# Optimization experiments

Hardware: AMD Instinct MI355X
Metric: run time of the kernel (lower is better)

## Reference

```python
import jax, jax.numpy as jnp
import numpy as np

SEGMENT_LENGTHS = [2048, 4096]
DILATION_RATES = [1, 2]


def _group_attention(qg, kg, vg, seg_len, r, gidx):
    # qg/kg/vg: [b, gh, n, d]; segmented dilated attention for one head group.
    b, gh, n, d = qg.shape
    nseg = n // seg_len
    scale = float(1.0 / np.sqrt(d))
    qs = qg.reshape(b, gh, nseg, seg_len, d)
    ks = kg.reshape(b, gh, nseg, seg_len, d)
    vs = vg.reshape(b, gh, nseg, seg_len, d)
    if r > 1:
        m = seg_len // r
        # offset = (group_idx + seg_idx) % r; pattern = offset + r*arange(m) (no wrap since seg_len % r == 0)
        offsets = (gidx + jnp.arange(nseg)) % r            # [nseg]
        idx = offsets[:, None] + r * jnp.arange(m)[None, :]  # [nseg, m]
        si = jnp.arange(nseg)[:, None]                      # [nseg, 1]
        qd = qs[:, :, si, idx]                              # [b, gh, nseg, m, d]
        kd = ks[:, :, si, idx]
        vd = vs[:, :, si, idx]
    else:
        qd, kd, vd = qs, ks, vs
    scores = jnp.einsum('bgsqd,bgskd->bgsqk', qd, kd) * scale
    attn = jax.nn.softmax(scores, axis=-1)
    out = jnp.einsum('bgsqk,bgskd->bgsqd', attn, vd)
    if r > 1:
        # scatter dilated outputs back to their segment positions; unselected positions stay 0
        full = jnp.zeros((b, gh, nseg, seg_len, d), dtype=qg.dtype)
        out = full.at[:, :, si, idx].set(out)
    return out.reshape(b, gh, n, d)


def reference(q, k, v):
    # q, k, v: [b, n, h, d]; ring_size == 1 -> single-device dilated attention
    b, n, h, d = q.shape
    ngroups = len(SEGMENT_LENGTHS)
    gsize = h // ngroups
    qt = jnp.transpose(q, (0, 2, 1, 3))  # [b, h, n, d]
    kt = jnp.transpose(k, (0, 2, 1, 3))
    vt = jnp.transpose(v, (0, 2, 1, 3))
    outs = []
    for i, (s, r) in enumerate(zip(SEGMENT_LENGTHS, DILATION_RATES)):
        hs, he = i * gsize, (i + 1) * gsize
        outs.append(_group_attention(qt[:, hs:he], kt[:, hs:he], vt[:, hs:he], s, r, i))
    out = jnp.concatenate(outs, axis=1)   # [b, h, n, d]
    return jnp.transpose(out, (0, 2, 1, 3))  # [b, n, h, d]


def setup_inputs() -> dict:
    key = jax.random.key(0)
    kq, kk, kv = jax.random.split(key, 3)
    shape = (1, 8192, 16, 128)
    return {
        'q': jax.random.normal(kq, shape, dtype=jnp.float32),
        'k': jax.random.normal(kk, shape, dtype=jnp.float32),
        'v': jax.random.normal(kv, shape, dtype=jnp.float32),
    }
```

## Files before the change

### kernel.cpp

```cpp
#include <hip/hip_runtime.h>
#include <hip/hip_bf16.h>

typedef __attribute__((ext_vector_type(8)))  short bf16x8;
typedef __attribute__((ext_vector_type(4)))  float f32x4;
typedef __attribute__((ext_vector_type(16))) float f32x16;
typedef __attribute__((ext_vector_type(4)))  int   int4v;

__device__ __forceinline__ short f2bf(float f) {
    unsigned u = __builtin_bit_cast(unsigned, f);
    unsigned r = u + 0x7fffu + ((u >> 16) & 1u);
    return (short)(r >> 16);
}

__device__ __forceinline__ int row_map(int p, int j) {
    if (p < 32) return (p & 3) * 2048 + j;
    return ((p - 32) & 1) == 0 ? (2 * j + 1) : (4096 + 2 * j);
}
__device__ __forceinline__ int head_of(int p) {
    return (p < 32) ? (p >> 2) : (8 + ((p - 32) >> 1));
}

__global__ __launch_bounds__(256) void conv_k_kernel(
    const float* __restrict__ K, short* __restrict__ Kws)
{
    const int cid = blockIdx.x * 256 + threadIdx.x;
    const int p   = cid >> 15;
    const int rem = cid & 32767;
    const int row = rem >> 4;
    const int d8  = (rem & 15) << 3;
    const int g   = row_map(p, row);
    const float* src = K + ((size_t)(g * 16 + head_of(p))) * 128 + d8;
    bf16x8 o;
    #pragma unroll
    for (int e = 0; e < 8; ++e) o[e] = f2bf(src[e]);
    *(bf16x8*)(Kws + (((size_t)p * 2048 + row) << 7) + d8) = o;
}

__global__ __launch_bounds__(256) void conv_v_kernel(
    const float* __restrict__ V, short* __restrict__ Vws)
{
    __shared__ short T[128][72];
    const int p  = blockIdx.x >> 5;
    const int kb = blockIdx.x & 31;
    const int tid = threadIdx.x;
    const int h = head_of(p);
    #pragma unroll
    for (int it = 0; it < 4; ++it) {
        const int cid  = it * 256 + tid;
        const int krow = cid & 63;
        const int d8   = (cid >> 6) << 3;
        const int g = row_map(p, kb * 64 + krow);
        const float* vp = V + ((size_t)(g * 16 + h)) * 128 + d8;
        #pragma unroll
        for (int e = 0; e < 8; ++e) T[d8 + e][krow] = f2bf(vp[e]);
    }
    __syncthreads();
    #pragma unroll
    for (int it = 0; it < 4; ++it) {
        const int j   = it * 256 + tid;
        const int d   = j >> 3;
        const int c16 = j & 7;
        bf16x8 val = *(const bf16x8*)&T[d][c16 * 8];
        *(bf16x8*)(Vws + ((size_t)p * 128 + d) * 2048 + kb * 64 + c16 * 8) = val;
    }
}

__global__ __launch_bounds__(256, 2) void dilated_attn7_kernel(
    const float* __restrict__ Q, const short* __restrict__ Kws,
    const short* __restrict__ Vws, float* __restrict__ O)
{
    __shared__ short Ks[64 * 128];
    __shared__ short Vt[128 * 64];
    __shared__ float sbuf[4][32];

    const int logical = (blockIdx.x & 7) * 96 + (blockIdx.x >> 3);
    const int pid  = logical >> 4;
    const int tile = logical & 15;
    const int h    = head_of(pid);

    const int tid  = threadIdx.x;
    const int wave = tid >> 6;
    const int lane = tid & 63;
    const int ql   = lane & 31;
    const int hi   = lane >> 5;

    const float scale_log2e = 0.08838834764831845f * 1.4426950408889634f;

    const short* Kp = Kws + ((size_t)pid * 2048 << 7);
    const short* Vp = Vws + ((size_t)pid * 128) * 2048;

    bf16x8 qf[8];
    {
        const int j = tile * 128 + wave * 32 + ql;
        const int g = row_map(pid, j);
        const float* qp = Q + ((size_t)(g * 16 + h)) * 128 + hi * 8;
        #pragma unroll
        for (int c = 0; c < 8; ++c) {
            bf16x8 f;
            #pragma unroll
            for (int e = 0; e < 8; ++e) f[e] = f2bf(qp[c * 16 + e] * scale_log2e);
            qf[c] = f;
        }
    }

    f32x16 oacc[4];
    #pragma unroll
    for (int dt = 0; dt < 4; ++dt) oacc[dt] = (f32x16)0.f;
    float m = -3.0e38f, l = 0.f;

    int4v kreg[4], vreg[4];

    auto LOADR = [&](int kb) {
        #pragma unroll
        for (int it = 0; it < 4; ++it) {
            const int j   = it * 256 + wave * 64 + lane;
            const int row = j >> 4;
            const int u   = j & 15;
            kreg[it] = *(const int4v*)(Kp + (((size_t)(kb * 64 + row)) << 7) + u * 8);
        }
        #pragma unroll
        for (int it = 0; it < 4; ++it) {
            const int j   = it * 256 + wave * 64 + lane;
            const int row = j >> 3;
            const int u   = j & 7;
            vreg[it] = *(const int4v*)(Vp + (size_t)row * 2048 + kb * 64 + u * 8);
        }
    };
    auto WRITE = [&]() {
        #pragma unroll
        for (int it = 0; it < 4; ++it) {
            const int j   = it * 256 + wave * 64 + lane;
            const int row = j >> 4;
            const int u   = j & 15;
            *(int4v*)&Ks[row * 128 + ((u ^ (row & 15)) << 3)] = kreg[it];
        }
        #pragma unroll
        for (int it = 0; it < 4; ++it) {
            const int j   = it * 256 + wave * 64 + lane;
            const int row = j >> 3;
            const int u   = j & 7;
            *(int4v*)&Vt[row * 64 + ((u ^ (row & 7)) << 3)] = vreg[it];
        }
    };

    LOADR(0);
    WRITE();
    __syncthreads();

    for (int t = 0; t < 32; ++t) {
        if (t < 31) LOADR(t + 1);

        f32x16 p[2];
        #pragma unroll
        for (int kt2 = 0; kt2 < 2; ++kt2) {
            f32x16 acc = (f32x16)0.f;
            const int row = kt2 * 32 + ql;
            #pragma unroll
            for (int c = 0; c < 8; ++c) {
                const int u = 2 * c + hi;
                bf16x8 a = *(const bf16x8*)&Ks[row * 128 + ((u ^ (row & 15)) << 3)];
                acc = __builtin_amdgcn_mfma_f32_32x32x16_bf16(a, qf[c], acc, 0, 0, 0);
            }
            p[kt2] = acc;
        }

        float rm = p[0][0];
        #pragma unroll
        for (int kt2 = 0; kt2 < 2; ++kt2)
            #pragma unroll
            for (int r = 0; r < 16; ++r) rm = fmaxf(rm, p[kt2][r]);
        rm = fmaxf(rm, __shfl_xor(rm, 32));

        if (__any(rm > m + 8.0f)) {
            const float mn = fmaxf(m, rm);
            const float sf = exp2f(m - mn);
            m = mn;
            l *= sf;
            if (lane < 32) sbuf[wave][lane] = sf;
            #pragma unroll
            for (int r = 0; r < 16; ++r) {
                const float s = sbuf[wave][(r & 3) + 8 * (r >> 2) + 4 * hi];
                #pragma unroll
                for (int dt = 0; dt < 4; ++dt) oacc[dt][r] *= s;
            }
        }

        float rs = 0.f;
        #pragma unroll
        for (int kt2 = 0; kt2 < 2; ++kt2)
            #pragma unroll
            for (int r = 0; r < 16; ++r) {
                const float pv = exp2f(p[kt2][r] - m);
                p[kt2][r] = pv;
                rs += pv;
            }
        rs += __shfl_xor(rs, 32);
        l += rs;

        bf16x8 pa[4];
        #pragma unroll
        for (int kt2 = 0; kt2 < 2; ++kt2) {
            int A0, A1, B0, B1, C0, C1, D0, D1;
            asm("v_cvt_pk_bf16_f32 %0,%1,%2" : "=v"(A0) : "v"(p[kt2][0]),  "v"(p[kt2][1]));
            asm("v_cvt_pk_bf16_f32 %0,%1,%2" : "=v"(A1) : "v"(p[kt2][2]),  "v"(p[kt2][3]));
            asm("v_cvt_pk_bf16_f32 %0,%1,%2" : "=v"(B0) : "v"(p[kt2][4]),  "v"(p[kt2][5]));
            asm("v_cvt_pk_bf16_f32 %0,%1,%2" : "=v"(B1) : "v"(p[kt2][6]),  "v"(p[kt2][7]));
            asm("v_cvt_pk_bf16_f32 %0,%1,%2" : "=v"(C0) : "v"(p[kt2][8]),  "v"(p[kt2][9]));
            asm("v_cvt_pk_bf16_f32 %0,%1,%2" : "=v"(C1) : "v"(p[kt2][10]), "v"(p[kt2][11]));
            asm("v_cvt_pk_bf16_f32 %0,%1,%2" : "=v"(D0) : "v"(p[kt2][12]), "v"(p[kt2][13]));
            asm("v_cvt_pk_bf16_f32 %0,%1,%2" : "=v"(D1) : "v"(p[kt2][14]), "v"(p[kt2][15]));
            asm("v_permlane32_swap_b32 %0, %1" : "+v"(A0), "+v"(B0));
            asm("v_permlane32_swap_b32 %0, %1" : "+v"(A1), "+v"(B1));
            asm("v_permlane32_swap_b32 %0, %1" : "+v"(C0), "+v"(D0));
            asm("v_permlane32_swap_b32 %0, %1" : "+v"(C1), "+v"(D1));
            pa[2 * kt2 + 0] = __builtin_bit_cast(bf16x8, (int4v){A0, A1, B0, B1});
            pa[2 * kt2 + 1] = __builtin_bit_cast(bf16x8, (int4v){C0, C1, D0, D1});
        }

        #pragma unroll
        for (int ks = 0; ks < 4; ++ks) {
            #pragma unroll
            for (int dt = 0; dt < 4; ++dt) {
                const int row = dt * 32 + ql;
                const int u   = 2 * ks + hi;
                bf16x8 vb = *(const bf16x8*)&Vt[row * 64 + ((u ^ (row & 7)) << 3)];
                oacc[dt] = __builtin_amdgcn_mfma_f32_32x32x16_bf16(pa[ks], vb, oacc[dt], 0, 0, 0);
            }
        }

        if (t < 31) {
            __syncthreads();
            WRITE();
            __syncthreads();
        }
    }

    if (lane < 32) sbuf[wave][lane] = 1.f / l;
    #pragma unroll
    for (int r = 0; r < 16; ++r) {
        const int qrow = (r & 3) + 8 * (r >> 2) + 4 * hi;
        const float inv = sbuf[wave][qrow];
        const int j = tile * 128 + wave * 32 + qrow;
        const int g = row_map(pid, j);
        float* op = O + ((size_t)(g * 16 + h)) * 128 + ql;
        #pragma unroll
        for (int dt = 0; dt < 4; ++dt)
            op[dt * 32] = oacc[dt][r] * inv;
    }
}

__global__ __launch_bounds__(256) void zero_fill_kernel(float* __restrict__ O)
{
    const int t = blockIdx.x * 256 + threadIdx.x;
    const int c4   = t & 31;
    const int rowi = (t >> 5) & 4095;
    const int hh   = t >> 17;
    const int row  = (rowi < 2048) ? (2 * rowi) : (4096 + 2 * (rowi - 2048) + 1);
    float4 z; z.x = 0.f; z.y = 0.f; z.z = 0.f; z.w = 0.f;
    *(float4*)&O[((size_t)(row * 16) + 8 + hh) * 128 + c4 * 4] = z;
}

#define BK    64
#define KPAD  136
#define VPAD  72
__global__ __launch_bounds__(256) void dilated_attn_v1_kernel(
    const float* __restrict__ Q, const float* __restrict__ K,
    const float* __restrict__ V, float* __restrict__ O)
{
    __shared__ short KsL[BK][KPAD];
    __shared__ short VtL[128][VPAD];
    __shared__ short PsL[4][16][VPAD];
    const int bid  = blockIdx.x;
    const int p    = bid >> 5;
    const int tile = bid & 31;
    const int h    = head_of(p);
    const int tid  = threadIdx.x;
    const int wave = tid >> 6;
    const int lane = tid & 63;
    const int lr   = lane & 15;
    const int lg   = lane >> 4;
    const float scale_log2e = 0.08838834764831845f * 1.4426950408889634f;
    bf16x8 qf[4];
    {
        const int j = tile * 64 + wave * 16 + lr;
        const int g = row_map(p, j);
        const float* qp = Q + ((size_t)(g * 16 + h)) * 128 + lg * 8;
        #pragma unroll
        for (int c = 0; c < 4; ++c) {
            bf16x8 f;
            #pragma unroll
            for (int e = 0; e < 8; ++e) f[e] = f2bf(qp[c * 32 + e] * scale_log2e);
            qf[c] = f;
        }
    }
    f32x4 oacc[8];
    #pragma unroll
    for (int i = 0; i < 8; ++i) oacc[i] = (f32x4)0.f;
    float m[4], l[4];
    #pragma unroll
    for (int r = 0; r < 4; ++r) { m[r] = -3.0e38f; l[r] = 0.f; }
    for (int kb = 0; kb < 2048 / BK; ++kb) {
        __syncthreads();
        #pragma unroll
        for (int it = 0; it < 4; ++it) {
            const int cid  = it * 256 + tid;
            const int krow = cid >> 4;
            const int dcol = (cid & 15) << 3;
            const int g = row_map(p, kb * BK + krow);
            const float* kp = K + ((size_t)(g * 16 + h)) * 128 + dcol;
            bf16x8 kk;
            #pragma unroll
            for (int e = 0; e < 8; ++e) kk[e] = f2bf(kp[e]);
            *(bf16x8*)&KsL[krow][dcol] = kk;
        }
        #pragma unroll
        for (int it = 0; it < 4; ++it) {
            const int cid  = it * 256 + tid;
            const int krow = cid & 63;
            const int dcol = (cid >> 6) << 3;
            const int g = row_map(p, kb * BK + krow);
            const float* vp = V + ((size_t)(g * 16 + h)) * 128 + dcol;
            #pragma unroll
            for (int e = 0; e < 8; ++e) VtL[dcol + e][krow] = f2bf(vp[e]);
        }
        __syncthreads();
        f32x4 s[4];
        #pragma unroll
        for (int t = 0; t < 4; ++t) {
            f32x4 acc = (f32x4)0.f;
            #pragma unroll
            for (int c = 0; c < 4; ++c) {
                bf16x8 b = *(const bf16x8*)&KsL[t * 16 + lr][c * 32 + lg * 8];
                acc = __builtin_amdgcn_mfma_f32_16x16x32_bf16(qf[c], b, acc, 0, 0, 0);
            }
            s[t] = acc;
        }
        #pragma unroll
        for (int r = 0; r < 4; ++r) {
            float bm = fmaxf(fmaxf(s[0][r], s[1][r]), fmaxf(s[2][r], s[3][r]));
            bm = fmaxf(bm, __shfl_xor(bm, 1));
            bm = fmaxf(bm, __shfl_xor(bm, 2));
            bm = fmaxf(bm, __shfl_xor(bm, 4));
            bm = fmaxf(bm, __shfl_xor(bm, 8));
            const float mn = fmaxf(m[r], bm);
            const float sf = exp2f(m[r] - mn);
            m[r] = mn;
            float rs = 0.f;
            #pragma unroll
            for (int t = 0; t < 4; ++t) {
                const float pv = exp2f(s[t][r] - mn);
                s[t][r] = pv;
                rs += pv;
            }
            rs += __shfl_xor(rs, 1);
            rs += __shfl_xor(rs, 2);
            rs += __shfl_xor(rs, 4);
            rs += __shfl_xor(rs, 8);
            l[r] = l[r] * sf + rs;
            #pragma unroll
            for (int dt = 0; dt < 8; ++dt) oacc[dt][r] *= sf;
        }
        #pragma unroll
        for (int t = 0; t < 4; ++t)
            #pragma unroll
            for (int r = 0; r < 4; ++r)
                PsL[wave][lg * 4 + r][t * 16 + lr] = f2bf(s[t][r]);
        #pragma unroll
        for (int cc = 0; cc < 2; ++cc) {
            bf16x8 pa = *(const bf16x8*)&PsL[wave][lr][cc * 32 + lg * 8];
            #pragma unroll
            for (int dt = 0; dt < 8; ++dt) {
                bf16x8 vb = *(const bf16x8*)&VtL[dt * 16 + lr][cc * 32 + lg * 8];
                oacc[dt] = __builtin_amdgcn_mfma_f32_16x16x32_bf16(pa, vb, oacc[dt], 0, 0, 0);
            }
        }
    }
    #pragma unroll
    for (int r = 0; r < 4; ++r) {
        const int j = tile * 64 + wave * 16 + lg * 4 + r;
        const int g = row_map(p, j);
        const float inv = 1.f / l[r];
        float* op = O + ((size_t)(g * 16 + h)) * 128 + lr;
        #pragma unroll
        for (int dt = 0; dt < 8; ++dt)
            op[dt * 16] = oacc[dt][r] * inv;
    }
}

extern "C" void kernel_launch(void* const* d_in, const int* in_sizes, int n_in,
                              void* d_out, int out_size, void* d_ws, size_t ws_size,
                              hipStream_t stream) {
    const float* q = (const float*)d_in[0];
    const float* k = (const float*)d_in[1];
    const float* v = (const float*)d_in[2];
    float* o = (float*)d_out;

    const size_t kws_elems = (size_t)48 * 2048 * 128;
    const size_t need = kws_elems * 2 * 2;
    hipLaunchKernelGGL(zero_fill_kernel, dim3(4096), dim3(256), 0, stream, o);
    if (ws_size >= need) {
        short* kws = (short*)d_ws;
        short* vws = kws + kws_elems;
        hipLaunchKernelGGL(conv_k_kernel, dim3(6144), dim3(256), 0, stream, k, kws);
        hipLaunchKernelGGL(conv_v_kernel, dim3(1536), dim3(256), 0, stream, v, vws);
        hipLaunchKernelGGL(dilated_attn7_kernel, dim3(48 * 16), dim3(256), 0, stream,
                           q, kws, vws, o);
    } else {
        hipLaunchKernelGGL(dilated_attn_v1_kernel, dim3(48 * 32), dim3(256), 0, stream,
                           q, k, v, o);
    }
}
```

Baseline: 181.0 us.

## Load V tiles straight into double-buffered LDS via global_load_lds

V tiles now go directly from global memory into a double-buffered LDS array using the global_load_lds builtin, with the XOR swizzle applied on the source address, so they no longer pass through registers. K still uses register staging into a single buffer. This frees vector registers, and launch bounds are raised from 2 to 3 blocks per CU to try for more occupancy. The trade-offs are more LDS per block and a full vmcnt(0) wait before each barrier, which also waits on the K loads.

```diff
diff --git a/kernel.cpp b/kernel.cpp
--- a/kernel.cpp
+++ b/kernel.cpp
@@ -19,6 +19,11 @@
 __device__ __forceinline__ int head_of(int p) {
     return (p < 32) ? (p >> 2) : (8 + ((p - 32) >> 1));
 }
+
+#define GLDS(gsrc, ldst)                                                          \
+    __builtin_amdgcn_global_load_lds(                                             \
+        (const __attribute__((address_space(1))) unsigned int*)(gsrc),            \
+        (__attribute__((address_space(3))) unsigned int*)(ldst), 16, 0, 0)
 
 __global__ __launch_bounds__(256) void conv_k_kernel(
     const float* __restrict__ K, short* __restrict__ Kws)
@@ -65,12 +70,12 @@
     }
 }
 
-__global__ __launch_bounds__(256, 2) void dilated_attn7_kernel(
+__global__ __launch_bounds__(256, 3) void dilated_attn8_kernel(
     const float* __restrict__ Q, const short* __restrict__ Kws,
     const short* __restrict__ Vws, float* __restrict__ O)
 {
     __shared__ short Ks[64 * 128];
-    __shared__ short Vt[128 * 64];
+    __shared__ short Vt[2][128 * 64];
     __shared__ float sbuf[4][32];
 
     const int logical = (blockIdx.x & 7) * 96 + (blockIdx.x >> 3);
@@ -108,9 +113,19 @@
     for (int dt = 0; dt < 4; ++dt) oacc[dt] = (f32x16)0.f;
     float m = -3.0e38f, l = 0.f;
 
-    int4v kreg[4], vreg[4];
-
-    auto LOADR = [&](int kb) {
+    int4v kreg[4];
+
+    auto GLDS_V = [&](int buf, int kb) {
+        #pragma unroll
+        for (int it = 0; it < 4; ++it) {
+            const int j   = it * 256 + wave * 64 + lane;
+            const int row = j >> 3;
+            const int u   = j & 7;
+            GLDS(Vp + (size_t)row * 2048 + kb * 64 + ((u ^ (row & 7)) << 3),
+                 &Vt[buf][(it * 256 + wave * 64) * 8]);
+        }
+    };
+    auto LOADK = [&](int kb) {
         #pragma unroll
         for (int it = 0; it < 4; ++it) {
             const int j   = it * 256 + wave * 64 + lane;
@@ -118,15 +133,8 @@
             const int u   = j & 15;
             kreg[it] = *(const int4v*)(Kp + (((size_t)(kb * 64 + row)) << 7) + u * 8);
         }
-        #pragma unroll
-        for (int it = 0; it < 4; ++it) {
-            const int j   = it * 256 + wave * 64 + lane;
-            const int row = j >> 3;
-            const int u   = j & 7;
-            vreg[it] = *(const int4v*)(Vp + (size_t)row * 2048 + kb * 64 + u * 8);
-        }
     };
-    auto WRITE = [&]() {
+    auto WRITEK = [&]() {
         #pragma unroll
         for (int it = 0; it < 4; ++it) {
             const int j   = it * 256 + wave * 64 + lane;
@@ -134,21 +142,20 @@
             const int u   = j & 15;
             *(int4v*)&Ks[row * 128 + ((u ^ (row & 15)) << 3)] = kreg[it];
         }
-        #pragma unroll
-        for (int it = 0; it < 4; ++it) {
-            const int j   = it * 256 + wave * 64 + lane;
-            const int row = j >> 3;
-            const int u   = j & 7;
-            *(int4v*)&Vt[row * 64 + ((u ^ (row & 7)) << 3)] = vreg[it];
-        }
     };
 
-    LOADR(0);
-    WRITE();
+    GLDS_V(0, 0);
+    LOADK(0);
+    WRITEK();
+    asm volatile("s_waitcnt vmcnt(0)" ::: "memory");
     __syncthreads();
 
     for (int t = 0; t < 32; ++t) {
-        if (t < 31) LOADR(t + 1);
+        const int cur = t & 1;
+        if (t < 31) {
+            GLDS_V(cur ^ 1, t + 1);
+            LOADK(t + 1);
+        }
 
         f32x16 p[2];
         #pragma unroll
@@ -223,14 +230,15 @@
             for (int dt = 0; dt < 4; ++dt) {
                 const int row = dt * 32 + ql;
                 const int u   = 2 * ks + hi;
-                bf16x8 vb = *(const bf16x8*)&Vt[row * 64 + ((u ^ (row & 7)) << 3)];
+                bf16x8 vb = *(const bf16x8*)&Vt[cur][row * 64 + ((u ^ (row & 7)) << 3)];
                 oacc[dt] = __builtin_amdgcn_mfma_f32_32x32x16_bf16(pa[ks], vb, oacc[dt], 0, 0, 0);
             }
         }
 
         if (t < 31) {
             __syncthreads();
-            WRITE();
+            WRITEK();
+            asm volatile("s_waitcnt vmcnt(0)" ::: "memory");
             __syncthreads();
         }
     }
@@ -403,7 +411,7 @@
         short* vws = kws + kws_elems;
         hipLaunchKernelGGL(conv_k_kernel, dim3(6144), dim3(256), 0, stream, k, kws);
         hipLaunchKernelGGL(conv_v_kernel, dim3(1536), dim3(256), 0, stream, v, vws);
-        hipLaunchKernelGGL(dilated_attn7_kernel, dim3(48 * 16), dim3(256), 0, stream,
+        hipLaunchKernelGGL(dilated_attn8_kernel, dim3(48 * 16), dim3(256), 0, stream,
                            q, kws, vws, o);
     } else {
         hipLaunchKernelGGL(dilated_attn_v1_kernel, dim3(48 * 32), dim3(256), 0, stream,
```

Measured after the change: 350.8 us. +93.8%, slower.
